# Optimization experiments

Hardware: AMD Instinct MI355X
Metric: run time of the kernel (lower is better)

Reference implementation:

```python
import jax, jax.numpy as jnp
import numpy as np

AUG_DIMS = 8
ODE_STEPS = 20  # fixed-step RK4 over t in [0, 1]


def _augment(x):
    # concat zeros along last (channel) dim: [B, S, F] -> [B, S, F + AUG_DIMS]
    z = jnp.zeros(x.shape[:-1] + (AUG_DIMS,), dtype=x.dtype)
    return jnp.concatenate([x, z], axis=-1)


def _ode_solve(z0, W, b):
    # dz/dt = z @ W.T + b, integrated with RK4, 20 steps, t: 0 -> 1
    h = 1.0 / ODE_STEPS

    def f(z):
        return z @ W.T + b

    def step(z, _):
        k1 = f(z)
        k2 = f(z + 0.5 * h * k1)
        k3 = f(z + 0.5 * h * k2)
        k4 = f(z + h * k3)
        z = z + (h / 6.0) * (k1 + 2.0 * k2 + 2.0 * k3 + k4)
        return z, None

    z_final, _ = jax.lax.scan(step, z0, None, length=ODE_STEPS)
    return z_final


def setup_inputs() -> dict:
    key = jax.random.key(0)
    ks = jax.random.split(key, 7)
    F_, C_, H_ = 76, 5, 128
    D = F_ + AUG_DIMS  # 84
    x = jax.random.normal(ks[0], (32, 2048, F_), dtype=jnp.float32)
    s = 1.0 / np.sqrt(D)
    W_ode = jax.random.uniform(ks[1], (D, D), minval=-s, maxval=s, dtype=jnp.float32)
    b_ode = jax.random.uniform(ks[2], (D,), minval=-s, maxval=s, dtype=jnp.float32)
    W_pen = jax.random.uniform(ks[3], (H_, D), minval=-s, maxval=s, dtype=jnp.float32)
    b_pen = jax.random.uniform(ks[4], (H_,), minval=-s, maxval=s, dtype=jnp.float32)
    sh = 1.0 / np.sqrt(H_)
    W_fin = jax.random.uniform(ks[5], (C_, H_), minval=-sh, maxval=sh, dtype=jnp.float32)
    b_fin = jax.random.uniform(ks[6], (C_,), minval=-sh, maxval=sh, dtype=jnp.float32)
    return {"x": x, "W_ode": W_ode, "b_ode": b_ode, "W_pen": W_pen,
            "b_pen": b_pen, "W_fin": W_fin, "b_fin": b_fin}


def reference(x, W_ode, b_ode, W_pen, b_pen, W_fin, b_fin):
    z0 = _augment(x)                       # [B, S, 84]
    z = _ode_solve(z0, W_ode, b_ode)       # ODE solve
    z = z + z0                             # skip-add of augmented input
    h = jax.nn.relu(z @ W_pen.T + b_pen)   # [B, S, 128]
    return h @ W_fin.T + b_fin             # [B, S, 5]
```

## Files before the change

### kernel.cpp

```cpp
#include <hip/hip_runtime.h>

#define K_IN 76
#define DD 84
#define HCH 128
#define CCH 5

#define NCOL 128

#define OFF_U 0
#define OFF_C (K_IN*HCH)

__device__ __constant__ float CU6[6] = {
    1.f, 0.5f, 1.f/6.f, 1.f/24.f, 1.f/120.f, 1.f/720.f };
__device__ __constant__ float CC6[6] = {
    0.5f, 1.f/6.f, 1.f/24.f, 1.f/120.f, 1.f/720.f, 1.f/5040.f };

__global__ __launch_bounds__(128) void col_kernel(
    const float* __restrict__ W,
    const float* __restrict__ bode,
    const float* __restrict__ Wpen,
    const float* __restrict__ bpen,
    float* __restrict__ ws)
{
    __shared__ __align__(16) float Sa[88];
    __shared__ __align__(16) float Sb[88];

    const int tid = threadIdx.x;
    const int j   = blockIdx.x;
    const bool act = (tid < DD);

    float wcol[DD];
    if (act) {
#pragma unroll
        for (int k = 0; k < DD; ++k) wcol[k] = W[k*DD + tid];
    }

    float s0 = 0.f, b = 0.f;
    if (act) {
        s0 = Wpen[j*DD + tid];
        b  = bode[tid];
        Sa[tid] = s0;
    }
    __syncthreads();

    float uacc = 2.f*s0, cacc = s0;

    const float* Sc = Sa;
    float*       Sn = Sb;
#pragma unroll
    for (int n = 0; n < 6; ++n) {
        float d = 0.f;
        if (act) {
            float a0 = 0.f, a1 = 0.f, a2 = 0.f, a3 = 0.f;
#pragma unroll
            for (int mg = 0; mg < 21; ++mg) {
                const float4 sv = *(const float4*)&Sc[mg*4];
                a0 = fmaf(sv.x, wcol[mg*4+0], a0);
                a1 = fmaf(sv.y, wcol[mg*4+1], a1);
                a2 = fmaf(sv.z, wcol[mg*4+2], a2);
                a3 = fmaf(sv.w, wcol[mg*4+3], a3);
            }
            d = (a0 + a1) + (a2 + a3);
            Sn[tid] = d;
        }
        __syncthreads();
        if (act) {
            uacc = fmaf(CU6[n], d, uacc);
            cacc = fmaf(CC6[n], d, cacc);
        }
        { float* t = (float*)Sc; Sc = Sn; Sn = t; }
    }

    if (tid < K_IN) ws[OFF_U + tid*HCH + j] = uacc;

    if (act) Sn[tid] = b * cacc;
    __syncthreads();
    if (tid < 64) {
        float v = Sn[tid] + ((tid < 20) ? Sn[64 + tid] : 0.f);
#pragma unroll
        for (int off = 32; off > 0; off >>= 1)
            v += __shfl_down(v, off, 64);
        if (tid == 0) ws[OFF_C + j] = bpen[j] + v;
    }
}

__global__ __launch_bounds__(256) void main_kernel(
    const float* __restrict__ x,
    const float* __restrict__ Ug,
    const float* __restrict__ cg,
    const float* __restrict__ Wfin,
    const float* __restrict__ bfin,
    float* __restrict__ out)
{
    __shared__ float Ut[K_IN*HCH];
    __shared__ float xs[128*K_IN];
    __shared__ float Vl[CCH*HCH];

    const int tid = threadIdx.x;
    const int tx = tid & 31, ty = tid >> 5;
    const int T0 = blockIdx.x * 128;

    for (int i = tid; i < (K_IN*HCH)/4; i += 256)
        ((float4*)Ut)[i] = ((const float4*)Ug)[i];
    {
        const float4* xg = (const float4*)(x + (size_t)T0 * K_IN);
        for (int i = tid; i < (128*K_IN)/4; i += 256)
            ((float4*)xs)[i] = xg[i];
    }
    for (int i = tid; i < CCH*HCH; i += 256) Vl[i] = Wfin[i];
    __syncthreads();

    const int j0 = tx*4;
    const int tb = ty*16;
    float acc[16][4];
#pragma unroll
    for (int t = 0; t < 16; ++t)
#pragma unroll
        for (int q = 0; q < 4; ++q) acc[t][q] = 0.f;

    for (int kc = 0; kc < 19; ++kc) {
        const float4 u0 = *(const float4*)&Ut[(4*kc+0)*HCH + j0];
        const float4 u1 = *(const float4*)&Ut[(4*kc+1)*HCH + j0];
        const float4 u2 = *(const float4*)&Ut[(4*kc+2)*HCH + j0];
        const float4 u3 = *(const float4*)&Ut[(4*kc+3)*HCH + j0];
#pragma unroll
        for (int ti = 0; ti < 16; ++ti) {
            const float4 xv = *(const float4*)&xs[(tb+ti)*K_IN + 4*kc];
            acc[ti][0] = fmaf(xv.x, u0.x, acc[ti][0]);
            acc[ti][1] = fmaf(xv.x, u0.y, acc[ti][1]);
            acc[ti][2] = fmaf(xv.x, u0.z, acc[ti][2]);
            acc[ti][3] = fmaf(xv.x, u0.w, acc[ti][3]);
            acc[ti][0] = fmaf(xv.y, u1.x, acc[ti][0]);
            acc[ti][1] = fmaf(xv.y, u1.y, acc[ti][1]);
            acc[ti][2] = fmaf(xv.y, u1.z, acc[ti][2]);
            acc[ti][3] = fmaf(xv.y, u1.w, acc[ti][3]);
            acc[ti][0] = fmaf(xv.z, u2.x, acc[ti][0]);
            acc[ti][1] = fmaf(xv.z, u2.y, acc[ti][1]);
            acc[ti][2] = fmaf(xv.z, u2.z, acc[ti][2]);
            acc[ti][3] = fmaf(xv.z, u2.w, acc[ti][3]);
            acc[ti][0] = fmaf(xv.w, u3.x, acc[ti][0]);
            acc[ti][1] = fmaf(xv.w, u3.y, acc[ti][1]);
            acc[ti][2] = fmaf(xv.w, u3.z, acc[ti][2]);
            acc[ti][3] = fmaf(xv.w, u3.w, acc[ti][3]);
        }
    }

    const float4 cv = *(const float4*)&cg[j0];
    float* opp = xs;
    float* opf = Ut;
    __syncthreads();

    for (int tg = 0; tg < 4; ++tg) {
        float oa[20];
#pragma unroll
        for (int s = 0; s < 4; ++s) {
            const int ti = tg*4 + s;
            const float h0 = fmaxf(acc[ti][0] + cv.x, 0.f);
            const float h1 = fmaxf(acc[ti][1] + cv.y, 0.f);
            const float h2 = fmaxf(acc[ti][2] + cv.z, 0.f);
            const float h3 = fmaxf(acc[ti][3] + cv.w, 0.f);
#pragma unroll
            for (int m = 0; m < CCH; ++m)
                oa[s*5+m] = h0*Vl[m*HCH + j0]     + h1*Vl[m*HCH + j0 + 1]
                          + h2*Vl[m*HCH + j0 + 2] + h3*Vl[m*HCH + j0 + 3];
        }
#pragma unroll
        for (int i = 0; i < 20; ++i) opp[tid*21 + i] = oa[i];
        __syncthreads();
        if (tid < 160) {
            const int typ = tid / 20, rem = tid % 20;
            float s = 0.f;
            for (int xx = 0; xx < 32; ++xx)
                s += opp[(typ*32 + xx)*21 + rem];
            opf[(typ*16 + tg*4)*5 + rem] = s;
        }
        __syncthreads();
    }

    if (tid < 160) {
        const int gi = tid*4;
        float4 v = *(const float4*)&opf[gi];
        v.x += bfin[(gi+0) % 5]; v.y += bfin[(gi+1) % 5];
        v.z += bfin[(gi+2) % 5]; v.w += bfin[(gi+3) % 5];
        *(float4*)&out[(size_t)T0*CCH + gi] = v;
    }
}

extern "C" void kernel_launch(void* const* d_in, const int* in_sizes, int n_in,
                              void* d_out, int out_size, void* d_ws, size_t ws_size,
                              hipStream_t stream)
{
    (void)in_sizes; (void)n_in; (void)out_size; (void)ws_size;
    const float* x    = (const float*)d_in[0];
    const float* Wode = (const float*)d_in[1];
    const float* bode = (const float*)d_in[2];
    const float* Wpen = (const float*)d_in[3];
    const float* bpen = (const float*)d_in[4];
    const float* Wfin = (const float*)d_in[5];
    const float* bfin = (const float*)d_in[6];
    float* out = (float*)d_out;
    float* wsf = (float*)d_ws;

    col_kernel<<<dim3(NCOL), dim3(128), 0, stream>>>(Wode, bode, Wpen, bpen, wsf);
    main_kernel<<<dim3(512), dim3(256), 0, stream>>>(x, wsf + OFF_U, wsf + OFF_C,
                                                     Wfin, bfin, out);
}
```

Baseline: 32.83 us.

## Fuse weight-precompute and main kernels with a global atomic flag handoff

```diff
diff --git a/kernel.cpp b/kernel.cpp
--- a/kernel.cpp
+++ b/kernel.cpp
@@ -6,110 +6,124 @@
 #define CCH 5
 
 #define NCOL 128
+#define NGRID 512
 
 #define OFF_U 0
 #define OFF_C (K_IN*HCH)
+#define OFF_FLAG 9856
 
 __device__ __constant__ float CU6[6] = {
     1.f, 0.5f, 1.f/6.f, 1.f/24.f, 1.f/120.f, 1.f/720.f };
 __device__ __constant__ float CC6[6] = {
     0.5f, 1.f/6.f, 1.f/24.f, 1.f/120.f, 1.f/720.f, 1.f/5040.f };
 
-__global__ __launch_bounds__(128) void col_kernel(
+__global__ __launch_bounds__(256) void fused_kernel(
+    const float* __restrict__ x,
     const float* __restrict__ W,
     const float* __restrict__ bode,
     const float* __restrict__ Wpen,
     const float* __restrict__ bpen,
-    float* __restrict__ ws)
-{
-    __shared__ __align__(16) float Sa[88];
-    __shared__ __align__(16) float Sb[88];
-
-    const int tid = threadIdx.x;
-    const int j   = blockIdx.x;
-    const bool act = (tid < DD);
-
-    float wcol[DD];
-    if (act) {
-#pragma unroll
-        for (int k = 0; k < DD; ++k) wcol[k] = W[k*DD + tid];
-    }
-
-    float s0 = 0.f, b = 0.f;
-    if (act) {
-        s0 = Wpen[j*DD + tid];
-        b  = bode[tid];
-        Sa[tid] = s0;
-    }
-    __syncthreads();
-
-    float uacc = 2.f*s0, cacc = s0;
-
-    const float* Sc = Sa;
-    float*       Sn = Sb;
-#pragma unroll
-    for (int n = 0; n < 6; ++n) {
-        float d = 0.f;
-        if (act) {
-            float a0 = 0.f, a1 = 0.f, a2 = 0.f, a3 = 0.f;
-#pragma unroll
-            for (int mg = 0; mg < 21; ++mg) {
-                const float4 sv = *(const float4*)&Sc[mg*4];
-                a0 = fmaf(sv.x, wcol[mg*4+0], a0);
-                a1 = fmaf(sv.y, wcol[mg*4+1], a1);
-                a2 = fmaf(sv.z, wcol[mg*4+2], a2);
-                a3 = fmaf(sv.w, wcol[mg*4+3], a3);
-            }
-            d = (a0 + a1) + (a2 + a3);
-            Sn[tid] = d;
-        }
-        __syncthreads();
-        if (act) {
-            uacc = fmaf(CU6[n], d, uacc);
-            cacc = fmaf(CC6[n], d, cacc);
-        }
-        { float* t = (float*)Sc; Sc = Sn; Sn = t; }
-    }
-
-    if (tid < K_IN) ws[OFF_U + tid*HCH + j] = uacc;
-
-    if (act) Sn[tid] = b * cacc;
-    __syncthreads();
-    if (tid < 64) {
-        float v = Sn[tid] + ((tid < 20) ? Sn[64 + tid] : 0.f);
-#pragma unroll
-        for (int off = 32; off > 0; off >>= 1)
-            v += __shfl_down(v, off, 64);
-        if (tid == 0) ws[OFF_C + j] = bpen[j] + v;
-    }
-}
-
-__global__ __launch_bounds__(256) void main_kernel(
-    const float* __restrict__ x,
-    const float* __restrict__ Ug,
-    const float* __restrict__ cg,
     const float* __restrict__ Wfin,
     const float* __restrict__ bfin,
-    float* __restrict__ out)
+    float* __restrict__ out,
+    float* __restrict__ ws,
+    unsigned* __restrict__ flag)
 {
     __shared__ float Ut[K_IN*HCH];
     __shared__ float xs[128*K_IN];
     __shared__ float Vl[CCH*HCH];
 
     const int tid = threadIdx.x;
-    const int tx = tid & 31, ty = tid >> 5;
-    const int T0 = blockIdx.x * 128;
-
-    for (int i = tid; i < (K_IN*HCH)/4; i += 256)
-        ((float4*)Ut)[i] = ((const float4*)Ug)[i];
+    const int bid = blockIdx.x;
+    const int T0 = bid * 128;
+
+    if (bid < NCOL) {
+        float* Sa = Ut;
+        float* Sb = Ut + 96;
+        const bool act = (tid < DD);
+
+        float wcol[DD];
+        float s0 = 0.f, b = 0.f;
+        if (act) {
+#pragma unroll
+            for (int k = 0; k < DD; ++k) wcol[k] = W[k*DD + tid];
+            s0 = Wpen[bid*DD + tid];
+            b  = bode[tid];
+            Sa[tid] = s0;
+        }
+        __syncthreads();
+
+        float uacc = 2.f*s0, cacc = s0;
+        const float* Sc = Sa;
+        float*       Sn = Sb;
+#pragma unroll
+        for (int n = 0; n < 6; ++n) {
+            float d = 0.f;
+            if (act) {
+                float a0 = 0.f, a1 = 0.f, a2 = 0.f, a3 = 0.f;
+#pragma unroll
+                for (int mg = 0; mg < 21; ++mg) {
+                    const float4 sv = *(const float4*)&Sc[mg*4];
+                    a0 = fmaf(sv.x, wcol[mg*4+0], a0);
+                    a1 = fmaf(sv.y, wcol[mg*4+1], a1);
+                    a2 = fmaf(sv.z, wcol[mg*4+2], a2);
+                    a3 = fmaf(sv.w, wcol[mg*4+3], a3);
+                }
+                d = (a0 + a1) + (a2 + a3);
+                Sn[tid] = d;
+            }
+            __syncthreads();
+            if (act) {
+                uacc = fmaf(CU6[n], d, uacc);
+                cacc = fmaf(CC6[n], d, cacc);
+            }
+            float* t = (float*)Sc; Sc = Sn; Sn = t;
+        }
+
+        if (tid < K_IN) ws[OFF_U + tid*HCH + bid] = uacc;
+        if (act) Sn[tid] = b * cacc;
+        __syncthreads();
+        if (tid < 64) {
+            float v = Sn[tid] + ((tid < 20) ? Sn[64 + tid] : 0.f);
+#pragma unroll
+            for (int off = 32; off > 0; off >>= 1)
+                v += __shfl_down(v, off, 64);
+            if (tid == 0) {
+                ws[OFF_C + bid] = bpen[bid] + v;
+                __threadfence();
+                __hip_atomic_fetch_add(flag, 1u, __ATOMIC_RELEASE,
+                                       __HIP_MEMORY_SCOPE_AGENT);
+            }
+        }
+    }
+
     {
         const float4* xg = (const float4*)(x + (size_t)T0 * K_IN);
         for (int i = tid; i < (128*K_IN)/4; i += 256)
             ((float4*)xs)[i] = xg[i];
-    }
-    for (int i = tid; i < CCH*HCH; i += 256) Vl[i] = Wfin[i];
+        for (int i = tid; i < CCH*HCH; i += 256) Vl[i] = Wfin[i];
+    }
+
+    if (tid == 0) {
+        int guard = 0;
+        while (__hip_atomic_load(flag, __ATOMIC_ACQUIRE,
+                                 __HIP_MEMORY_SCOPE_AGENT) < NCOL) {
+            __builtin_amdgcn_s_sleep(8);
+            if (++guard > (1<<16)) break;
+        }
+    }
     __syncthreads();
-
+    {
+        unsigned fv = __hip_atomic_load(flag, __ATOMIC_ACQUIRE,
+                                        __HIP_MEMORY_SCOPE_AGENT);
+        asm volatile("" :: "v"(fv));
+    }
+
+    for (int i = tid; i < (K_IN*HCH)/4; i += 256)
+        ((float4*)Ut)[i] = ((const float4*)(ws + OFF_U))[i];
+    __syncthreads();
+
+    const int tx = tid & 31, ty = tid >> 5;
     const int j0 = tx*4;
     const int tb = ty*16;
     float acc[16][4];
@@ -145,7 +159,7 @@
         }
     }
 
-    const float4 cv = *(const float4*)&cg[j0];
+    const float4 cv = *(const float4*)&(ws + OFF_C)[j0];
     float* opp = xs;
     float* opf = Ut;
     __syncthreads();
@@ -200,8 +214,9 @@
     const float* bfin = (const float*)d_in[6];
     float* out = (float*)d_out;
     float* wsf = (float*)d_ws;
-
-    col_kernel<<<dim3(NCOL), dim3(128), 0, stream>>>(Wode, bode, Wpen, bpen, wsf);
-    main_kernel<<<dim3(512), dim3(256), 0, stream>>>(x, wsf + OFF_U, wsf + OFF_C,
-                                                     Wfin, bfin, out);
+    unsigned* flag = (unsigned*)(wsf + OFF_FLAG);
+
+    hipMemsetAsync(flag, 0, 64, stream);
+    fused_kernel<<<dim3(NGRID), dim3(256), 0, stream>>>(
+        x, Wode, bode, Wpen, bpen, Wfin, bfin, out, wsf, flag);
 }
```

New measurement: 72.23 us. 2.2x slower.
